# Kernel tuning notes

Hardware: AMD Instinct MI355X
Metric: run time of the kernel (lower is better)

The kernel has to match this reference:

```python
import jax, jax.numpy as jnp
import numpy as np

D_MODEL = 1024
N_HEADS = 16
N_KV = 4
HEAD_DIM = 64
R = 256
B, N = 2, 2048


def setup_inputs() -> dict:
    key = jax.random.key(0)
    ks = jax.random.split(key, 5)
    x = jax.random.normal(ks[0], (B, N, D_MODEL), jnp.float32)
    # rotary cos/sin table: (N, HEAD_DIM//2, 2)
    inv = 1.0 / (10000.0 ** (jnp.arange(0, HEAD_DIM, 2, dtype=jnp.float32) / HEAD_DIM))
    ang = jnp.arange(N, dtype=jnp.float32)[:, None] * inv[None, :]
    freqs_cis = jnp.stack([jnp.cos(ang), jnp.sin(ang)], axis=-1)
    s = 0.02
    Wq = jax.random.normal(ks[1], (D_MODEL, N_HEADS * HEAD_DIM), jnp.float32) * s
    Wk = jax.random.normal(ks[2], (D_MODEL, N_KV * HEAD_DIM), jnp.float32) * s
    Wv = jax.random.normal(ks[3], (D_MODEL, N_KV * HEAD_DIM), jnp.float32) * s
    Wo = jax.random.normal(ks[4], (N_HEADS * HEAD_DIM, D_MODEL), jnp.float32) * s
    return dict(x=x, freqs_cis=freqs_cis, Wq=Wq, Wk=Wk, Wv=Wv, Wo=Wo)


def _select_pairs(scores_i, best_b_i, r):
    """Greedy top-r pair selection with unique-b constraint (one batch row)."""
    half = scores_i.shape[0]
    order = jnp.argsort(-scores_i)  # descending by best similarity

    def step(carry, a_local):
        used, count = carry
        b_local = best_b_i[a_local]
        take = jnp.logical_and(jnp.logical_not(used[b_local]), count < r)
        used = used.at[b_local].set(used[b_local] | take)
        count = count + take.astype(jnp.int32)
        return (used, count), (take, a_local.astype(jnp.int32), b_local.astype(jnp.int32))

    (_, count), (takes, a_locs, b_locs) = jax.lax.scan(
        step, (jnp.zeros(half, bool), jnp.int32(0)), order)
    pos = jnp.cumsum(takes.astype(jnp.int32)) - 1
    idx = jnp.where(takes, pos, r)  # dump non-taken into slot r
    sel_a = jnp.zeros(r + 1, jnp.int32).at[idx].set(a_locs)[:r]
    sel_b = jnp.zeros(r + 1, jnp.int32).at[idx].set(b_locs)[:r]
    valid = jnp.arange(r) < count  # pad (if fewer than r unique) with first pair
    sel_a = jnp.where(valid, sel_a, sel_a[0])
    sel_b = jnp.where(valid, sel_b, sel_b[0])
    return sel_a, sel_b


def bipartite_indices(metric, r):
    """Returns (global_a, global_b, keep_idx) for merge/unmerge."""
    Bm, Nm, _ = metric.shape
    a = metric[:, 0::2]  # (B, half, C)
    b = metric[:, 1::2]
    an = a / jnp.maximum(jnp.linalg.norm(a, axis=-1, keepdims=True), 1e-12)
    bn = b / jnp.maximum(jnp.linalg.norm(b, axis=-1, keepdims=True), 1e-12)
    scores = jnp.einsum('bic,bjc->bij', an, bn)  # (B, half, half)
    best_scores = scores.max(axis=2)
    best_b = scores.argmax(axis=2)
    sel_a, sel_b = jax.vmap(lambda s, m: _select_pairs(s, m, r))(best_scores, best_b)
    global_a = 2 * sel_a      # even indices
    global_b = 2 * sel_b + 1  # odd indices
    bidx = jnp.arange(Bm)[:, None]
    keep_mask = jnp.ones((Bm, Nm), bool).at[bidx, global_b].set(False)
    # stable argsort puts kept (False) positions first, in original order
    keep_idx = jnp.argsort(~keep_mask, axis=1)[:, :Nm - r]
    return global_a, global_b, keep_idx


def merge(x, global_a, global_b, keep_idx):
    Bm = x.shape[0]
    bidx = jnp.arange(Bm)[:, None]
    xa = jnp.take_along_axis(x, global_a[..., None], axis=1)
    xb = jnp.take_along_axis(x, global_b[..., None], axis=1)
    x_out = x.at[bidx, global_a].set((xa + xb) * 0.5)
    return jnp.take_along_axis(x_out, keep_idx[..., None], axis=1)


def unmerge(xm, global_a, global_b, keep_idx, n_orig):
    Bm, _, C = xm.shape
    bidx = jnp.arange(Bm)[:, None]
    out = jnp.zeros((Bm, n_orig, C), xm.dtype).at[bidx, keep_idx].set(xm)
    xa = jnp.take_along_axis(out, global_a[..., None], axis=1)
    return out.at[bidx, global_b].set(xa)


def _rope(t, freqs):
    # t: (B, N, H, HD), freqs: (N, HD//2, 2)
    cos = freqs[None, :, None, :, 0]
    sin = freqs[None, :, None, :, 1]
    t1 = t[..., 0::2]
    t2 = t[..., 1::2]
    rot = jnp.stack([t1 * cos - t2 * sin, t1 * sin + t2 * cos], axis=-1)
    return rot.reshape(t.shape)


def _attention(x_m, freqs, Wq, Wk, Wv, Wo):
    Bm, Nm, _ = x_m.shape
    q = (x_m @ Wq).reshape(Bm, Nm, N_HEADS, HEAD_DIM)
    k = (x_m @ Wk).reshape(Bm, Nm, N_KV, HEAD_DIM)
    v = (x_m @ Wv).reshape(Bm, Nm, N_KV, HEAD_DIM)
    q = _rope(q, freqs)
    k = _rope(k, freqs)
    rep = N_HEADS // N_KV
    k = jnp.repeat(k, rep, axis=2)
    v = jnp.repeat(v, rep, axis=2)
    att = jnp.einsum('bqhd,bkhd->bhqk', q, k) / np.sqrt(HEAD_DIM).astype(np.float32)
    w = jax.nn.softmax(att, axis=-1)
    o = jnp.einsum('bhqk,bkhd->bqhd', w, v).reshape(Bm, Nm, N_HEADS * HEAD_DIM)
    return o @ Wo


def reference(x, freqs_cis, Wq, Wk, Wv, Wo):
    n = x.shape[1]
    metric = jax.lax.stop_gradient(x @ Wk)  # k_proj under no_grad
    ga, gb, ki = bipartite_indices(metric, R)
    x_m = merge(x, ga, gb, ki)
    n_merged = x_m.shape[1]
    out_m = _attention(x_m, freqs_cis[:n_merged], Wq, Wk, Wv, Wo)
    return unmerge(out_m, ga, gb, ki, n)
```

## Files before the change

kernel.cpp:

```cpp
#include <hip/hip_runtime.h>
#include <hip/hip_bf16.h>
#include <math.h>

#define BB 2
#define NN 2048
#define DM 1024
#define NH 16
#define NKV 4
#define HD 64
#define RR 256
#define HALF 1024
#define NM 1792
#define NT 28
#define NSPL 4

typedef __bf16 bf16x8 __attribute__((ext_vector_type(8)));
typedef float f32x4 __attribute__((ext_vector_type(4)));

__device__ inline unsigned pk2(float a, float b) {
  union { __bf16 h; unsigned short u; } ua, ub;
  ua.h = (__bf16)a;
  ub.h = (__bf16)b;
  return (unsigned)ua.u | ((unsigned)ub.u << 16);
}

__device__ inline unsigned shu(unsigned v, int s) {
  return (unsigned)__shfl((int)v, s, 64);
}

__global__ __launch_bounds__(256) void gemm_bf16(
    const __bf16* __restrict__ A, const __bf16* __restrict__ Bt,
    float* __restrict__ C, int M, int N, int K) {
  __shared__ __align__(16) __bf16 As[4096];
  __shared__ __align__(16) __bf16 Bs[4096];
  const int bm0 = blockIdx.x * 64;
  const int bn0 = blockIdx.y * 64;
  const int w = threadIdx.x >> 6;
  const int lane = threadIdx.x & 63;
  f32x4 acc[4];
#pragma unroll
  for (int nt = 0; nt < 4; ++nt) acc[nt] = (f32x4){0.f, 0.f, 0.f, 0.f};
  for (int kk = 0; kk < K; kk += 64) {
    __syncthreads();
#pragma unroll
    for (int t2 = threadIdx.x; t2 < 512; t2 += 256) {
      const int blk = t2 >> 7, s = (t2 >> 6) & 1, l = t2 & 63;
      const int kc = kk + s * 32 + ((l >> 4) << 3);
      *(float4*)&As[t2 * 8] =
          *(const float4*)(A + (size_t)(bm0 + blk * 16 + (l & 15)) * K + kc);
      *(float4*)&Bs[t2 * 8] =
          *(const float4*)(Bt + (size_t)(bn0 + blk * 16 + (l & 15)) * K + kc);
    }
    __syncthreads();
#pragma unroll
    for (int s = 0; s < 2; ++s) {
      bf16x8 a = *(const bf16x8*)&As[((w * 2 + s) * 64 + lane) * 8];
#pragma unroll
      for (int nt = 0; nt < 4; ++nt) {
        bf16x8 bfr = *(const bf16x8*)&Bs[((nt * 2 + s) * 64 + lane) * 8];
        acc[nt] =
            __builtin_amdgcn_mfma_f32_16x16x32_bf16(a, bfr, acc[nt], 0, 0, 0);
      }
    }
  }
  const int g = lane >> 4, ml = lane & 15;
#pragma unroll
  for (int nt = 0; nt < 4; ++nt)
#pragma unroll
    for (int r = 0; r < 4; ++r)
      C[(size_t)(bm0 + w * 16 + g * 4 + r) * N + bn0 + nt * 16 + ml] =
          acc[nt][r];
}

__global__ __launch_bounds__(256) void gemm_wo(
    const __bf16* __restrict__ A, const __bf16* __restrict__ Bt,
    const int* __restrict__ keep_idx, const int* __restrict__ dst2,
    float* __restrict__ out, int M, int N, int K) {
  __shared__ __align__(16) __bf16 As[4096];
  __shared__ __align__(16) __bf16 Bs[4096];
  const int bm0 = blockIdx.x * 64;
  const int bn0 = blockIdx.y * 64;
  const int w = threadIdx.x >> 6;
  const int lane = threadIdx.x & 63;
  f32x4 acc[4];
#pragma unroll
  for (int nt = 0; nt < 4; ++nt) acc[nt] = (f32x4){0.f, 0.f, 0.f, 0.f};
  for (int kk = 0; kk < K; kk += 64) {
    __syncthreads();
#pragma unroll
    for (int t2 = threadIdx.x; t2 < 512; t2 += 256) {
      const int blk = t2 >> 7, s = (t2 >> 6) & 1, l = t2 & 63;
      const int kc = kk + s * 32 + ((l >> 4) << 3);
      *(float4*)&As[t2 * 8] =
          *(const float4*)(A + (size_t)(bm0 + blk * 16 + (l & 15)) * K + kc);
      *(float4*)&Bs[t2 * 8] =
          *(const float4*)(Bt + (size_t)(bn0 + blk * 16 + (l & 15)) * K + kc);
    }
    __syncthreads();
#pragma unroll
    for (int s = 0; s < 2; ++s) {
      bf16x8 a = *(const bf16x8*)&As[((w * 2 + s) * 64 + lane) * 8];
#pragma unroll
      for (int nt = 0; nt < 4; ++nt) {
        bf16x8 bfr = *(const bf16x8*)&Bs[((nt * 2 + s) * 64 + lane) * 8];
        acc[nt] =
            __builtin_amdgcn_mfma_f32_16x16x32_bf16(a, bfr, acc[nt], 0, 0, 0);
      }
    }
  }
  const int g = lane >> 4, ml = lane & 15;
#pragma unroll
  for (int r = 0; r < 4; ++r) {
    const int row = bm0 + w * 16 + g * 4 + r;
    const int bb = row / NM, tt = row % NM;
    const int p1 = keep_idx[bb * NM + tt];
    const int p2 = dst2[bb * NM + tt];
#pragma unroll
    for (int nt = 0; nt < 4; ++nt) {
      const int col = bn0 + nt * 16 + ml;
      float v = acc[nt][r];
      out[((size_t)(bb * NN + p1)) * DM + col] = v;
      if (p2 >= 0) out[((size_t)(bb * NN + p2)) * DM + col] = v;
    }
  }
}

__global__ __launch_bounds__(256) void gemm3t(
    const __bf16* __restrict__ Ah, const __bf16* __restrict__ Al,
    const __bf16* __restrict__ Bh, const __bf16* __restrict__ Bl,
    float* __restrict__ C0, float* __restrict__ C1, int M, int N, int K) {
  __shared__ __align__(16) __bf16 Ahs[4096], Als[4096], Bhs[4096], Bls[4096];
  const int z = blockIdx.z;
  float* C = z ? C1 : C0;
  const int kof = z * (K / 2);
  const int bm0 = blockIdx.x * 64;
  const int bn0 = blockIdx.y * 64;
  const int w = threadIdx.x >> 6;
  const int lane = threadIdx.x & 63;
  f32x4 acc[4];
#pragma unroll
  for (int nt = 0; nt < 4; ++nt) acc[nt] = (f32x4){0.f, 0.f, 0.f, 0.f};
  for (int kk = kof; kk < kof + K / 2; kk += 64) {
    __syncthreads();
#pragma unroll
    for (int t2 = threadIdx.x; t2 < 512; t2 += 256) {
      const int blk = t2 >> 7, s = (t2 >> 6) & 1, l = t2 & 63;
      const size_t ra = (size_t)(bm0 + blk * 16 + (l & 15)) * K;
      const size_t rb = (size_t)(bn0 + blk * 16 + (l & 15)) * K;
      const int col = kk + s * 32 + ((l >> 4) << 3);
      *(float4*)&Ahs[t2 * 8] = *(const float4*)(Ah + ra + col);
      *(float4*)&Als[t2 * 8] = *(const float4*)(Al + ra + col);
      *(float4*)&Bhs[t2 * 8] = *(const float4*)(Bh + rb + col);
      *(float4*)&Bls[t2 * 8] = *(const float4*)(Bl + rb + col);
    }
    __syncthreads();
#pragma unroll
    for (int s = 0; s < 2; ++s) {
      bf16x8 ah = *(const bf16x8*)&Ahs[((w * 2 + s) * 64 + lane) * 8];
      bf16x8 al = *(const bf16x8*)&Als[((w * 2 + s) * 64 + lane) * 8];
#pragma unroll
      for (int nt = 0; nt < 4; ++nt) {
        bf16x8 bh = *(const bf16x8*)&Bhs[((nt * 2 + s) * 64 + lane) * 8];
        bf16x8 bl = *(const bf16x8*)&Bls[((nt * 2 + s) * 64 + lane) * 8];
        acc[nt] = __builtin_amdgcn_mfma_f32_16x16x32_bf16(al, bh, acc[nt], 0, 0, 0);
        acc[nt] = __builtin_amdgcn_mfma_f32_16x16x32_bf16(ah, bl, acc[nt], 0, 0, 0);
        acc[nt] = __builtin_amdgcn_mfma_f32_16x16x32_bf16(ah, bh, acc[nt], 0, 0, 0);
      }
    }
  }
  const int g = lane >> 4, ml = lane & 15;
#pragma unroll
  for (int nt = 0; nt < 4; ++nt)
#pragma unroll
    for (int r = 0; r < 4; ++r)
      C[(size_t)(bm0 + w * 16 + g * 4 + r) * N + bn0 + nt * 16 + ml] =
          acc[nt][r];
}

__global__ __launch_bounds__(256) void gemm_scam(
    const __bf16* __restrict__ Ah, const __bf16* __restrict__ Al,
    const __bf16* __restrict__ Bh, const __bf16* __restrict__ Bl,
    float* __restrict__ sval, int* __restrict__ sidx) {
  __shared__ __align__(16) __bf16 Ahs[4096], Als[4096], Bhs[4096], Bls[4096];
  const size_t zo = (size_t)blockIdx.z * HALF * 256;
  const int bm0 = blockIdx.x * 64;
  const int bn0 = blockIdx.y * 64;
  const int w = threadIdx.x >> 6;
  const int lane = threadIdx.x & 63;
  f32x4 acc[4];
#pragma unroll
  for (int nt = 0; nt < 4; ++nt) acc[nt] = (f32x4){0.f, 0.f, 0.f, 0.f};
  for (int kk = 0; kk < 256; kk += 64) {
    __syncthreads();
#pragma unroll
    for (int t2 = threadIdx.x; t2 < 512; t2 += 256) {
      const int blk = t2 >> 7, s = (t2 >> 6) & 1, l = t2 & 63;
      const size_t ra = zo + (size_t)(bm0 + blk * 16 + (l & 15)) * 256;
      const size_t rb = zo + (size_t)(bn0 + blk * 16 + (l & 15)) * 256;
      const int col = kk + s * 32 + ((l >> 4) << 3);
      *(float4*)&Ahs[t2 * 8] = *(const float4*)(Ah + ra + col);
      *(float4*)&Als[t2 * 8] = *(const float4*)(Al + ra + col);
      *(float4*)&Bhs[t2 * 8] = *(const float4*)(Bh + rb + col);
      *(float4*)&Bls[t2 * 8] = *(const float4*)(Bl + rb + col);
    }
    __syncthreads();
#pragma unroll
    for (int s = 0; s < 2; ++s) {
      bf16x8 ah = *(const bf16x8*)&Ahs[((w * 2 + s) * 64 + lane) * 8];
      bf16x8 al = *(const bf16x8*)&Als[((w * 2 + s) * 64 + lane) * 8];
#pragma unroll
      for (int nt = 0; nt < 4; ++nt) {
        bf16x8 bh = *(const bf16x8*)&Bhs[((nt * 2 + s) * 64 + lane) * 8];
        bf16x8 bl = *(const bf16x8*)&Bls[((nt * 2 + s) * 64 + lane) * 8];
        acc[nt] = __builtin_amdgcn_mfma_f32_16x16x32_bf16(al, bh, acc[nt], 0, 0, 0);
        acc[nt] = __builtin_amdgcn_mfma_f32_16x16x32_bf16(ah, bl, acc[nt], 0, 0, 0);
        acc[nt] = __builtin_amdgcn_mfma_f32_16x16x32_bf16(ah, bh, acc[nt], 0, 0, 0);
      }
    }
  }
  const int g = lane >> 4, ml = lane & 15;
#pragma unroll
  for (int r = 0; r < 4; ++r) {
    float bv = acc[0][r];
    int bc = bn0 + ml;
#pragma unroll
    for (int nt = 1; nt < 4; ++nt) {
      float v = acc[nt][r];
      int c = bn0 + nt * 16 + ml;
      if (v > bv) { bv = v; bc = c; }
    }
#pragma unroll
    for (int off = 1; off < 16; off <<= 1) {
      float vo = __shfl_xor(bv, off, 64);
      int co = __shfl_xor(bc, off, 64);
      if (vo > bv || (vo == bv && co < bc)) { bv = vo; bc = co; }
    }
    if (ml == 0) {
      const int row = bm0 + w * 16 + g * 4 + r;
      const size_t o = ((size_t)blockIdx.z * HALF + row) * 16 + (bn0 >> 6);
      sval[o] = bv;
      sidx[o] = bc;
    }
  }
}

__global__ __launch_bounds__(256) void argmax_reduce(
    const float* __restrict__ sval, const int* __restrict__ sidx,
    float* __restrict__ best_s, int* __restrict__ best_b) {
  const int lane = threadIdx.x & 63;
  const int e = lane & 15;
  const int rid = blockIdx.x * 16 + (threadIdx.x >> 6) * 4 + (lane >> 4);
  float bv = sval[rid * 16 + e];
  int bc = sidx[rid * 16 + e];
#pragma unroll
  for (int off = 1; off < 16; off <<= 1) {
    float vo = __shfl_xor(bv, off, 64);
    int co = __shfl_xor(bc, off, 64);
    if (vo > bv || (vo == bv && co < bc)) { bv = vo; bc = co; }
  }
  if (e == 0) {
    best_s[rid] = bv;
    best_b[rid] = bc;
  }
}

__global__ __launch_bounds__(256) void hilo_split(const float* __restrict__ x,
                                                  __bf16* __restrict__ xh,
                                                  __bf16* __restrict__ xl) {
  const int i = blockIdx.x * 256 + threadIdx.x;
  float4 v = ((const float4*)x)[i];
  float f[4] = {v.x, v.y, v.z, v.w};
  union { __bf16 h[4]; uint2 u; } H, L;
#pragma unroll
  for (int j = 0; j < 4; ++j) {
    __bf16 hh = (__bf16)f[j];
    H.h[j] = hh;
    L.h[j] = (__bf16)(f[j] - (float)hh);
  }
  ((uint2*)xh)[i] = H.u;
  ((uint2*)xl)[i] = L.u;
}

__global__ __launch_bounds__(256) void transpose_all(
    const float* __restrict__ Wq, const float* __restrict__ Wk,
    const float* __restrict__ Wv, const float* __restrict__ Wo,
    __bf16* __restrict__ Wqkvt, __bf16* __restrict__ Wktl,
    __bf16* __restrict__ Wot) {
  __shared__ float ld[64][65];
  const int z = blockIdx.x;
  const float* src;
  __bf16* dsth;
  __bf16* dstl = nullptr;
  int N, k0, n0, rowoff;
  if (z < 256) {
    src = Wq; N = 1024; k0 = (z >> 4) << 6; n0 = (z & 15) << 6;
    dsth = Wqkvt; rowoff = 0;
  } else if (z < 320) {
    int zz = z - 256;
    src = Wk; N = 256; k0 = (zz >> 2) << 6; n0 = (zz & 3) << 6;
    dsth = Wqkvt; rowoff = 1024; dstl = Wktl;
  } else if (z < 384) {
    int zz = z - 320;
    src = Wv; N = 256; k0 = (zz >> 2) << 6; n0 = (zz & 3) << 6;
    dsth = Wqkvt; rowoff = 1280;
  } else {
    int zz = z - 384;
    src = Wo; N = 1024; k0 = (zz >> 4) << 6; n0 = (zz & 15) << 6;
    dsth = Wot; rowoff = 0;
  }
  for (int i = threadIdx.x; i < 1024; i += 256) {
    int r = i >> 4, c4 = i & 15;
    float4 v = *(const float4*)(src + (size_t)(k0 + r) * N + n0 + c4 * 4);
    ld[r][c4 * 4 + 0] = v.x;
    ld[r][c4 * 4 + 1] = v.y;
    ld[r][c4 * 4 + 2] = v.z;
    ld[r][c4 * 4 + 3] = v.w;
  }
  __syncthreads();
  for (int i = threadIdx.x; i < 4096; i += 256) {
    int n = i >> 6, k = i & 63;
    float v = ld[k][n];
    __bf16 hh = (__bf16)v;
    dsth[(size_t)(rowoff + n0 + n) * 1024 + k0 + k] = hh;
    if (dstl)
      dstl[(size_t)(n0 + n) * 1024 + k0 + k] = (__bf16)(v - (float)hh);
  }
}

__global__ __launch_bounds__(256) void normalize_split(
    const float* __restrict__ m0, const float* __restrict__ m1,
    __bf16* __restrict__ anh, __bf16* __restrict__ anl,
    __bf16* __restrict__ bnh, __bf16* __restrict__ bnl) {
  const int row = blockIdx.x;
  const int b = row >> 11;
  const int r = row & 2047;
  const int t = threadIdx.x;
  float v = m0[(size_t)row * 256 + t] + m1[(size_t)row * 256 + t];
  float ss = v * v;
#pragma unroll
  for (int o = 32; o > 0; o >>= 1) ss += __shfl_xor(ss, o, 64);
  __shared__ float wsum[4];
  if ((t & 63) == 0) wsum[t >> 6] = ss;
  __syncthreads();
  float tot = wsum[0] + wsum[1] + wsum[2] + wsum[3];
  float inv = 1.f / fmaxf(sqrtf(tot), 1e-12f);
  float nv = v * inv;
  __bf16 hh = (__bf16)nv;
  __bf16 ll = (__bf16)(nv - (float)hh);
  size_t o = ((size_t)b * HALF + (r >> 1)) * 256 + t;
  if (r & 1) {
    bnh[o] = hh;
    bnl[o] = ll;
  } else {
    anh[o] = hh;
    anl[o] = ll;
  }
}

__global__ __launch_bounds__(512) void sort_desc(const float* __restrict__ best_s,
                                                 int* __restrict__ order) {
  const int b = blockIdx.x;
  __shared__ float sv[1024];
  __shared__ int si[1024];
  for (int i = threadIdx.x; i < 1024; i += 512) {
    sv[i] = best_s[b * HALF + i];
    si[i] = i;
  }
  __syncthreads();
  for (int k = 2; k <= 1024; k <<= 1) {
    for (int j = k >> 1; j > 0; j >>= 1) {
      for (int t = threadIdx.x; t < 1024; t += 512) {
        int ixj = t ^ j;
        if (ixj > t) {
          bool dir = ((t & k) == 0);
          float va = sv[t], vb = sv[ixj];
          int ia = si[t], ib = si[ixj];
          bool before = (vb > va) || (vb == va && ib < ia);
          if (before == dir) {
            sv[t] = vb; sv[ixj] = va;
            si[t] = ib; si[ixj] = ia;
          }
        }
      }
      __syncthreads();
    }
  }
  for (int i = threadIdx.x; i < 1024; i += 512) order[b * HALF + i] = si[i];
}

__global__ __launch_bounds__(256) void select_and_index(
    const int* __restrict__ best_b, const int* __restrict__ order,
    int* __restrict__ keep_idx, int* __restrict__ partner,
    int* __restrict__ dst2) {
  const int b = blockIdx.x;
  __shared__ int rankA[HALF];
  __shared__ int minrank[HALF];
  __shared__ int taken[HALF];
  __shared__ int sel_a[RR], sel_b[RR];
  __shared__ int removed[NN];
  __shared__ int src_row[NN];
  __shared__ int tsum[256];
  const int t = threadIdx.x;

  for (int i = t; i < HALF; i += 256) { minrank[i] = 0x7fffffff; taken[i] = 0; }
  for (int i = t; i < NN; i += 256) {
    removed[i] = 0;
    partner[b * NN + i] = -1;
  }
  for (int i = t; i < NM; i += 256) dst2[b * NM + i] = -1;
  __syncthreads();
  int ord[4];
#pragma unroll
  for (int q = 0; q < 4; ++q) {
    int step = t * 4 + q;
    ord[q] = order[b * HALF + step];
    rankA[ord[q]] = step;
  }
  __syncthreads();
#pragma unroll
  for (int q = 0; q < 4; ++q) {
    int a = t * 4 + q;
    atomicMin(&minrank[best_b[b * HALF + a]], rankA[a]);
  }
  __syncthreads();
  for (int i = t; i < HALF; i += 256) {
    int mr = minrank[i];
    if (mr != 0x7fffffff) taken[mr] = 1;
  }
  __syncthreads();
  int c[4];
  int mysum = 0;
#pragma unroll
  for (int q = 0; q < 4; ++q) { c[q] = taken[t * 4 + q]; mysum += c[q]; }
  tsum[t] = mysum;
  __syncthreads();
  for (int off = 1; off < 256; off <<= 1) {
    int v = (t >= off) ? tsum[t - off] : 0;
    __syncthreads();
    tsum[t] += v;
    __syncthreads();
  }
  int run = tsum[t] - mysum;
#pragma unroll
  for (int q = 0; q < 4; ++q) {
    if (c[q] && run < RR) {
      int a = ord[q];
      sel_a[run] = 2 * a;
      sel_b[run] = 2 * best_b[b * HALF + a] + 1;
    }
    run += c[q];
  }
  __syncthreads();
  const int cnt = min(tsum[255], RR);
  if (t >= cnt) { sel_a[t] = sel_a[0]; sel_b[t] = sel_b[0]; }
  __syncthreads();
  {
    int ga = sel_a[t], gb = sel_b[t];
    removed[gb] = 1;
    partner[b * NN + ga] = gb;
  }
  __syncthreads();
  int myc = 0;
#pragma unroll
  for (int q = 0; q < 8; ++q) myc += !removed[8 * t + q];
  tsum[t] = myc;
  __syncthreads();
  for (int off = 1; off < 256; off <<= 1) {
    int v = (t >= off) ? tsum[t - off] : 0;
    __syncthreads();
    tsum[t] += v;
    __syncthreads();
  }
  int pos = tsum[t] - myc;
#pragma unroll
  for (int q = 0; q < 8; ++q) {
    int p = 8 * t + q;
    int sr = -1;
    if (!removed[p]) {
      if (pos < NM) {
        keep_idx[b * NM + pos] = p;
        sr = pos;
      }
      ++pos;
    }
    src_row[p] = sr;
  }
  __syncthreads();
  {
    int sr = src_row[sel_a[t]];
    dst2[b * NM + sr] = sel_b[t];
  }
}

__global__ __launch_bounds__(256) void merge_kernel(
    const float* __restrict__ x, const int* __restrict__ keep_idx,
    const int* __restrict__ partner, __bf16* __restrict__ x_mb) {
  const int mrow = blockIdx.x;
  const int b = mrow / NM;
  const int t = mrow % NM;
  const int p = keep_idx[b * NM + t];
  const int pp = partner[b * NN + p];
  const float4* src =
      reinterpret_cast<const float4*>(x + ((size_t)b * NN + p) * DM);
  float4 val = src[threadIdx.x];
  if (pp >= 0) {
    const float4* s2 =
        reinterpret_cast<const float4*>(x + ((size_t)b * NN + pp) * DM);
    float4 v2 = s2[threadIdx.x];
    val.x = 0.5f * (val.x + v2.x);
    val.y = 0.5f * (val.y + v2.y);
    val.z = 0.5f * (val.z + v2.z);
    val.w = 0.5f * (val.w + v2.w);
  }
  union { __bf16 h[4]; uint2 u; } U;
  U.h[0] = (__bf16)val.x;
  U.h[1] = (__bf16)val.y;
  U.h[2] = (__bf16)val.z;
  U.h[3] = (__bf16)val.w;
  ((uint2*)(x_mb + (size_t)mrow * DM))[threadIdx.x] = U.u;
}

__global__ __launch_bounds__(256) void rope_fused(
    const float* __restrict__ qkv, const float* __restrict__ fc,
    __bf16* __restrict__ qbh, __bf16* __restrict__ kbh) {
  const int row = blockIdx.x;
  const int t = row % NM;
  const int b = row / NM;
  for (int idx = threadIdx.x; idx < 640; idx += 256) {
    int u = idx & 31;
    float c = fc[(t * 32 + u) * 2];
    float s = fc[(t * 32 + u) * 2 + 1];
    if (idx < 512) {
      int h = idx >> 5;
      const float* p = qkv + (size_t)row * 1536 + h * 64 + 2 * u;
      float x1 = p[0], x2 = p[1];
      __bf16* d = qbh + ((size_t)(b * NH + h) * NM + t) * 64 + 2 * u;
      d[0] = (__bf16)((x1 * c - x2 * s) * 0.125f);
      d[1] = (__bf16)((x1 * s + x2 * c) * 0.125f);
    } else {
      int h = (idx - 512) >> 5;
      const float* p = qkv + (size_t)row * 1536 + 1024 + h * 64 + 2 * u;
      float x1 = p[0], x2 = p[1];
      __bf16* d = kbh + ((size_t)(b * NKV + h) * NM + t) * 64 + 2 * u;
      d[0] = (__bf16)(x1 * c - x2 * s);
      d[1] = (__bf16)(x1 * s + x2 * c);
    }
  }
}

__global__ __launch_bounds__(256) void v_repack(const float* __restrict__ qkv,
                                                __bf16* __restrict__ vtb) {
  __shared__ float ld[64][65];
  int bid = blockIdx.x;
  const int kt = bid % (NM / 64); bid /= (NM / 64);
  const int kvh = bid % NKV;
  const int b = bid / NKV;
  const int j0 = kt * 64;
  for (int t2 = threadIdx.x; t2 < 1024; t2 += 256) {
    int key = t2 >> 4, c4 = t2 & 15;
    float4 v4 = *reinterpret_cast<const float4*>(
        qkv + (size_t)(b * NM + j0 + key) * 1536 + 1280 + kvh * 64 + c4 * 4);
    ld[key][c4 * 4 + 0] = v4.x;
    ld[key][c4 * 4 + 1] = v4.y;
    ld[key][c4 * 4 + 2] = v4.z;
    ld[key][c4 * 4 + 3] = v4.w;
  }
  __syncthreads();
  const int dim = threadIdx.x >> 2, kc = threadIdx.x & 3;
  __bf16* out = vtb + ((size_t)(b * NKV + kvh) * 64 + dim) * NM + j0 + kc * 16;
#pragma unroll
  for (int kk = 0; kk < 16; ++kk) out[kk] = (__bf16)ld[kc * 16 + kk][dim];
}

__global__ __launch_bounds__(512) void attn_mfma(
    const __bf16* __restrict__ qbh, const __bf16* __restrict__ kbh,
    const __bf16* __restrict__ vtb, float* __restrict__ pl,
    __bf16* __restrict__ pacc) {
  __shared__ __align__(16) __bf16 Ks[4096];
  __shared__ __align__(16) __bf16 Vs[4096];
  int bid = blockIdx.x;
  const int qt2 = bid % (NM / 32); bid /= (NM / 32);
  const int split = bid % NSPL; bid /= NSPL;
  const int kvh = bid % NKV;
  const int b = bid / NKV;
  const int w = threadIdx.x >> 6;
  const int lane = threadIdx.x & 63;
  const int h = kvh * 4 + (w & 3);
  const int qt = qt2 * 32 + (w >> 2) * 16;
  const int g = lane >> 4;
  const int ml = lane & 15;

  const __bf16* qrow = qbh + ((size_t)(b * NH + h) * NM + qt + ml) * 64;
  bf16x8 qa0 = *reinterpret_cast<const bf16x8*>(qrow + g * 8);
  bf16x8 qa1 = *reinterpret_cast<const bf16x8*>(qrow + 32 + g * 8);

  f32x4 acc[4];
#pragma unroll
  for (int mt = 0; mt < 4; ++mt) acc[mt] = (f32x4){0.f, 0.f, 0.f, 0.f};
  float lsum = 0.f;

  const __bf16* kp = kbh + (size_t)(b * NKV + kvh) * NM * 64;
  const __bf16* vp = vtb + (size_t)(b * NKV + kvh) * 64 * NM;
  const int src0 = ((lane >> 4) & 1) * 32 + ml;
  const int src1 = src0 + 16;
  const int sel = g >> 1;

  const int jt0 = split * (NT / NSPL);
  for (int jt = jt0; jt < jt0 + NT / NSPL; ++jt) {
    __syncthreads();
    {
      const int t2 = threadIdx.x;
      const int blk = t2 >> 7, s = (t2 >> 6) & 1, l = t2 & 63;
      *(float4*)&Ks[t2 * 8] = *(const float4*)(
          kp + (size_t)(jt * 64 + blk * 16 + (l & 15)) * 64 + s * 32 +
          ((l >> 4) << 3));
      *(float4*)&Vs[t2 * 8] = *(const float4*)(
          vp + (size_t)(blk * 16 + (l & 15)) * NM + jt * 64 + s * 32 +
          ((l >> 4) << 3));
    }
    __syncthreads();
    f32x4 S[4];
#pragma unroll
    for (int nt = 0; nt < 4; ++nt) {
      bf16x8 k0 = *(const bf16x8*)&Ks[(nt * 128 + lane) * 8];
      bf16x8 k1 = *(const bf16x8*)&Ks[(nt * 128 + 64 + lane) * 8];
      f32x4 s4 = (f32x4){0.f, 0.f, 0.f, 0.f};
      s4 = __builtin_amdgcn_mfma_f32_16x16x32_bf16(k0, qa0, s4, 0, 0, 0);
      s4 = __builtin_amdgcn_mfma_f32_16x16x32_bf16(k1, qa1, s4, 0, 0, 0);
      S[nt] = s4;
    }
    float p[4][4];
#pragma unroll
    for (int nt = 0; nt < 4; ++nt)
#pragma unroll
      for (int r = 0; r < 4; ++r) {
        p[nt][r] = __expf(S[nt][r]);
        lsum += p[nt][r];
      }
    unsigned pk[4][2];
#pragma unroll
    for (int nt = 0; nt < 4; ++nt) {
      pk[nt][0] = pk2(p[nt][0], p[nt][1]);
      pk[nt][1] = pk2(p[nt][2], p[nt][3]);
    }
    unsigned A00 = shu(pk[0][0], src0), A01 = shu(pk[0][1], src0);
    unsigned A10 = shu(pk[1][0], src0), A11 = shu(pk[1][1], src0);
    unsigned B00 = shu(pk[0][0], src1), B01 = shu(pk[0][1], src1);
    unsigned B10 = shu(pk[1][0], src1), B11 = shu(pk[1][1], src1);
    unsigned C00 = shu(pk[2][0], src0), C01 = shu(pk[2][1], src0);
    unsigned C10 = shu(pk[3][0], src0), C11 = shu(pk[3][1], src0);
    unsigned D00 = shu(pk[2][0], src1), D01 = shu(pk[2][1], src1);
    unsigned D10 = shu(pk[3][0], src1), D11 = shu(pk[3][1], src1);
    union { uint4 u; bf16x8 v; } P0, P1;
    P0.u.x = sel ? A10 : A00; P0.u.y = sel ? A11 : A01;
    P0.u.z = sel ? B10 : B00; P0.u.w = sel ? B11 : B01;
    P1.u.x = sel ? C10 : C00; P1.u.y = sel ? C11 : C01;
    P1.u.z = sel ? D10 : D00; P1.u.w = sel ? D11 : D01;
#pragma unroll
    for (int mt = 0; mt < 4; ++mt) {
      bf16x8 v0 = *(const bf16x8*)&Vs[(mt * 128 + lane) * 8];
      bf16x8 v1 = *(const bf16x8*)&Vs[(mt * 128 + 64 + lane) * 8];
      acc[mt] = __builtin_amdgcn_mfma_f32_16x16x32_bf16(v0, P0.v, acc[mt], 0, 0, 0);
      acc[mt] = __builtin_amdgcn_mfma_f32_16x16x32_bf16(v1, P1.v, acc[mt], 0, 0, 0);
    }
  }
  lsum += __shfl_xor(lsum, 16, 64);
  lsum += __shfl_xor(lsum, 32, 64);
  const size_t row = (size_t)(b * NH + h) * NM + qt + ml;
  if (g == 0) pl[row * NSPL + split] = lsum;
  __bf16* pa = pacc + (row * NSPL + split) * 64;
#pragma unroll
  for (int mt = 0; mt < 4; ++mt) {
    uint2 u;
    u.x = pk2(acc[mt][0], acc[mt][1]);
    u.y = pk2(acc[mt][2], acc[mt][3]);
    *reinterpret_cast<uint2*>(pa + mt * 16 + g * 4) = u;
  }
}

__global__ __launch_bounds__(256) void attn_combine(
    const float* __restrict__ pl, const __bf16* __restrict__ pacc,
    __bf16* __restrict__ attn_ob) {
  const size_t rid = (size_t)blockIdx.x * 4 + (threadIdx.x >> 6);
  const int d = threadIdx.x & 63;
  float num = 0.f, den = 0.f;
#pragma unroll
  for (int s = 0; s < NSPL; ++s) {
    num += (float)pacc[(rid * NSPL + s) * 64 + d];
    den += pl[rid * NSPL + s];
  }
  float o = num / den;
  const int q = (int)(rid % NM);
  const int h = (int)((rid / NM) % NH);
  const int b = (int)(rid / ((size_t)NM * NH));
  attn_ob[((size_t)(b * NM + q)) * DM + h * 64 + d] = (__bf16)o;
}

extern "C" void kernel_launch(void* const* d_in, const int* in_sizes, int n_in,
                              void* d_out, int out_size, void* d_ws,
                              size_t ws_size, hipStream_t stream) {
  const float* x = (const float*)d_in[0];
  const float* fc = (const float*)d_in[1];
  const float* Wq = (const float*)d_in[2];
  const float* Wk = (const float*)d_in[3];
  const float* Wv = (const float*)d_in[4];
  const float* Wo = (const float*)d_in[5];
  float* out = (float*)d_out;

  char* ws = (char*)d_ws;
  size_t off = 0;
  auto alloc = [&](size_t bytes) {
    void* p = ws + off;
    off += (bytes + 255) & ~(size_t)255;
    return p;
  };
  float* metric0 = (float*)alloc((size_t)BB * NN * 256 * 4);
  float* metric1 = (float*)alloc((size_t)BB * NN * 256 * 4);
  float* best_s = (float*)alloc((size_t)BB * HALF * 4);
  int* best_b = (int*)alloc((size_t)BB * HALF * 4);
  int* order = (int*)alloc((size_t)BB * HALF * 4);
  int* keep_idx = (int*)alloc((size_t)BB * NM * 4);
  int* partner = (int*)alloc((size_t)BB * NN * 4);
  int* dst2 = (int*)alloc((size_t)BB * NM * 4);
  float* sval = (float*)alloc((size_t)BB * HALF * 16 * 4);
  int* sidx = (int*)alloc((size_t)BB * HALF * 16 * 4);
  char* bigreg = (char*)alloc((size_t)30 * 1024 * 1024);
  __bf16* xh = (__bf16*)bigreg;
  __bf16* xl = (__bf16*)(bigreg + (size_t)8704 * 1024);
  __bf16* anh = (__bf16*)bigreg;
  __bf16* anl = (__bf16*)(bigreg + (size_t)1100 * 1024);
  __bf16* bnh = (__bf16*)(bigreg + (size_t)2200 * 1024);
  __bf16* bnl = (__bf16*)(bigreg + (size_t)3300 * 1024);
  float* qkv = (float*)bigreg;
  __bf16* pacc = (__bf16*)bigreg;
  __bf16* x_mb = (__bf16*)alloc((size_t)BB * NM * DM * 2);
  __bf16* qbh = (__bf16*)alloc((size_t)BB * NH * NM * 64 * 2);
  __bf16* kbh = (__bf16*)alloc((size_t)BB * NKV * NM * 64 * 2);
  __bf16* vtb = (__bf16*)alloc((size_t)BB * NKV * 64 * NM * 2);
  __bf16* attn_ob = (__bf16*)alloc((size_t)BB * NM * DM * 2);
  float* pl = (float*)alloc((size_t)BB * NH * NM * NSPL * 4);
  __bf16* Wqkvt = (__bf16*)alloc((size_t)1536 * DM * 2);
  __bf16* Wktl = (__bf16*)alloc((size_t)256 * DM * 2);
  __bf16* Wot = (__bf16*)alloc((size_t)DM * DM * 2);
  const __bf16* Wkth = Wqkvt + (size_t)1024 * 1024;

  transpose_all<<<640, 256, 0, stream>>>(Wq, Wk, Wv, Wo, Wqkvt, Wktl, Wot);
  hilo_split<<<(BB * NN * DM / 4) / 256, 256, 0, stream>>>(x, xh, xl);
  gemm3t<<<dim3(64, 4, 2), 256, 0, stream>>>(xh, xl, Wkth, Wktl, metric0,
                                             metric1, BB * NN, 256, DM);
  normalize_split<<<BB * NN, 256, 0, stream>>>(metric0, metric1, anh, anl, bnh,
                                               bnl);
  gemm_scam<<<dim3(16, 16, 2), 256, 0, stream>>>(anh, anl, bnh, bnl, sval,
                                                 sidx);
  argmax_reduce<<<(BB * HALF) / 16, 256, 0, stream>>>(sval, sidx, best_s,
                                                      best_b);
  sort_desc<<<BB, 512, 0, stream>>>(best_s, order);
  select_and_index<<<BB, 256, 0, stream>>>(best_b, order, keep_idx, partner,
                                           dst2);
  merge_kernel<<<BB * NM, 256, 0, stream>>>(x, keep_idx, partner, x_mb);
  gemm_bf16<<<dim3(56, 24), 256, 0, stream>>>(x_mb, Wqkvt, qkv, BB * NM, 1536,
                                              DM);
  rope_fused<<<BB * NM, 256, 0, stream>>>(qkv, fc, qbh, kbh);
  v_repack<<<BB * NKV * (NM / 64), 256, 0, stream>>>(qkv, vtb);
  attn_mfma<<<BB * NKV * NSPL * (NM / 32), 512, 0, stream>>>(qbh, kbh, vtb, pl,
                                                             pacc);
  attn_combine<<<(BB * NH * NM) / 4, 256, 0, stream>>>(pl, pacc, attn_ob);
  gemm_wo<<<dim3(56, 16), 256, 0, stream>>>(attn_ob, Wot, keep_idx, dst2, out,
                                            BB * NM, DM, DM);
}
```

Measured before the change: 306.6 us.

## Use async global-to-LDS loads and 128-row tiles in projection GEMMs

Replaces register-staged global-to-shared copies with `global_load_lds` direct-to-LDS transfers in all GEMM kernels and in the attention K/V tile loads. This is meant to remove the VGPR round trip and the extra LDS write instructions. The QKV and output-projection GEMMs also move to 128-row tiles with two accumulator sets per wave, so each B tile is reused twice and launch grids are halved. The trade-off is higher register and LDS use per block and fewer blocks to fill the GPU. There is still no double buffering, so load latency remains exposed behind the barriers.

```diff
diff --git a/kernel.cpp b/kernel.cpp
--- a/kernel.cpp
+++ b/kernel.cpp
@@ -28,101 +28,131 @@
   return (unsigned)__shfl((int)v, s, 64);
 }
 
+__device__ __forceinline__ void async16(const void* g, void* l) {
+  __builtin_amdgcn_global_load_lds(
+      (const __attribute__((address_space(1))) void*)g,
+      (__attribute__((address_space(3))) void*)l, 16, 0, 0);
+}
+
 __global__ __launch_bounds__(256) void gemm_bf16(
     const __bf16* __restrict__ A, const __bf16* __restrict__ Bt,
     float* __restrict__ C, int M, int N, int K) {
-  __shared__ __align__(16) __bf16 As[4096];
+  __shared__ __align__(16) __bf16 As[8192];
   __shared__ __align__(16) __bf16 Bs[4096];
-  const int bm0 = blockIdx.x * 64;
+  const int bm0 = blockIdx.x * 128;
   const int bn0 = blockIdx.y * 64;
   const int w = threadIdx.x >> 6;
   const int lane = threadIdx.x & 63;
-  f32x4 acc[4];
-#pragma unroll
-  for (int nt = 0; nt < 4; ++nt) acc[nt] = (f32x4){0.f, 0.f, 0.f, 0.f};
+  f32x4 acc[2][4];
+#pragma unroll
+  for (int i = 0; i < 2; ++i)
+#pragma unroll
+    for (int nt = 0; nt < 4; ++nt) acc[i][nt] = (f32x4){0.f, 0.f, 0.f, 0.f};
   for (int kk = 0; kk < K; kk += 64) {
     __syncthreads();
 #pragma unroll
-    for (int t2 = threadIdx.x; t2 < 512; t2 += 256) {
-      const int blk = t2 >> 7, s = (t2 >> 6) & 1, l = t2 & 63;
-      const int kc = kk + s * 32 + ((l >> 4) << 3);
-      *(float4*)&As[t2 * 8] =
-          *(const float4*)(A + (size_t)(bm0 + blk * 16 + (l & 15)) * K + kc);
-      *(float4*)&Bs[t2 * 8] =
-          *(const float4*)(Bt + (size_t)(bn0 + blk * 16 + (l & 15)) * K + kc);
+    for (int it = 0; it < 4; ++it) {
+      const int c = it * 256 + w * 64 + lane;
+      async16(A + (size_t)(bm0 + ((c >> 7) << 4) + (c & 15)) * K + kk +
+                  (((c >> 6) & 1) << 5) + (((c >> 4) & 3) << 3),
+              &As[(it * 256 + w * 64) * 8]);
+    }
+#pragma unroll
+    for (int it = 0; it < 2; ++it) {
+      const int c = it * 256 + w * 64 + lane;
+      async16(Bt + (size_t)(bn0 + ((c >> 7) << 4) + (c & 15)) * K + kk +
+                  (((c >> 6) & 1) << 5) + (((c >> 4) & 3) << 3),
+              &Bs[(it * 256 + w * 64) * 8]);
     }
     __syncthreads();
 #pragma unroll
     for (int s = 0; s < 2; ++s) {
-      bf16x8 a = *(const bf16x8*)&As[((w * 2 + s) * 64 + lane) * 8];
+      bf16x8 a0 = *(const bf16x8*)&As[((2 * w) * 128 + s * 64 + lane) * 8];
+      bf16x8 a1 = *(const bf16x8*)&As[((2 * w + 1) * 128 + s * 64 + lane) * 8];
 #pragma unroll
       for (int nt = 0; nt < 4; ++nt) {
-        bf16x8 bfr = *(const bf16x8*)&Bs[((nt * 2 + s) * 64 + lane) * 8];
-        acc[nt] =
-            __builtin_amdgcn_mfma_f32_16x16x32_bf16(a, bfr, acc[nt], 0, 0, 0);
+        bf16x8 bfr = *(const bf16x8*)&Bs[(nt * 128 + s * 64 + lane) * 8];
+        acc[0][nt] =
+            __builtin_amdgcn_mfma_f32_16x16x32_bf16(a0, bfr, acc[0][nt], 0, 0, 0);
+        acc[1][nt] =
+            __builtin_amdgcn_mfma_f32_16x16x32_bf16(a1, bfr, acc[1][nt], 0, 0, 0);
       }
     }
   }
   const int g = lane >> 4, ml = lane & 15;
 #pragma unroll
-  for (int nt = 0; nt < 4; ++nt)
-#pragma unroll
-    for (int r = 0; r < 4; ++r)
-      C[(size_t)(bm0 + w * 16 + g * 4 + r) * N + bn0 + nt * 16 + ml] =
-          acc[nt][r];
+  for (int i = 0; i < 2; ++i)
+#pragma unroll
+    for (int nt = 0; nt < 4; ++nt)
+#pragma unroll
+      for (int r = 0; r < 4; ++r)
+        C[(size_t)(bm0 + (2 * w + i) * 16 + g * 4 + r) * N + bn0 + nt * 16 +
+          ml] = acc[i][nt][r];
 }
 
 __global__ __launch_bounds__(256) void gemm_wo(
     const __bf16* __restrict__ A, const __bf16* __restrict__ Bt,
     const int* __restrict__ keep_idx, const int* __restrict__ dst2,
     float* __restrict__ out, int M, int N, int K) {
-  __shared__ __align__(16) __bf16 As[4096];
+  __shared__ __align__(16) __bf16 As[8192];
   __shared__ __align__(16) __bf16 Bs[4096];
-  const int bm0 = blockIdx.x * 64;
+  const int bm0 = blockIdx.x * 128;
   const int bn0 = blockIdx.y * 64;
   const int w = threadIdx.x >> 6;
   const int lane = threadIdx.x & 63;
-  f32x4 acc[4];
-#pragma unroll
-  for (int nt = 0; nt < 4; ++nt) acc[nt] = (f32x4){0.f, 0.f, 0.f, 0.f};
+  f32x4 acc[2][4];
+#pragma unroll
+  for (int i = 0; i < 2; ++i)
+#pragma unroll
+    for (int nt = 0; nt < 4; ++nt) acc[i][nt] = (f32x4){0.f, 0.f, 0.f, 0.f};
   for (int kk = 0; kk < K; kk += 64) {
     __syncthreads();
 #pragma unroll
-    for (int t2 = threadIdx.x; t2 < 512; t2 += 256) {
-      const int blk = t2 >> 7, s = (t2 >> 6) & 1, l = t2 & 63;
-      const int kc = kk + s * 32 + ((l >> 4) << 3);
-      *(float4*)&As[t2 * 8] =
-          *(const float4*)(A + (size_t)(bm0 + blk * 16 + (l & 15)) * K + kc);
-      *(float4*)&Bs[t2 * 8] =
-          *(const float4*)(Bt + (size_t)(bn0 + blk * 16 + (l & 15)) * K + kc);
+    for (int it = 0; it < 4; ++it) {
+      const int c = it * 256 + w * 64 + lane;
+      async16(A + (size_t)(bm0 + ((c >> 7) << 4) + (c & 15)) * K + kk +
+                  (((c >> 6) & 1) << 5) + (((c >> 4) & 3) << 3),
+              &As[(it * 256 + w * 64) * 8]);
+    }
+#pragma unroll
+    for (int it = 0; it < 2; ++it) {
+      const int c = it * 256 + w * 64 + lane;
+      async16(Bt + (size_t)(bn0 + ((c >> 7) << 4) + (c & 15)) * K + kk +
+                  (((c >> 6) & 1) << 5) + (((c >> 4) & 3) << 3),
+              &Bs[(it * 256 + w * 64) * 8]);
     }
     __syncthreads();
 #pragma unroll
     for (int s = 0; s < 2; ++s) {
-      bf16x8 a = *(const bf16x8*)&As[((w * 2 + s) * 64 + lane) * 8];
+      bf16x8 a0 = *(const bf16x8*)&As[((2 * w) * 128 + s * 64 + lane) * 8];
+      bf16x8 a1 = *(const bf16x8*)&As[((2 * w + 1) * 128 + s * 64 + lane) * 8];
 #pragma unroll
       for (int nt = 0; nt < 4; ++nt) {
-        bf16x8 bfr = *(const bf16x8*)&Bs[((nt * 2 + s) * 64 + lane) * 8];
-        acc[nt] =
-            __builtin_amdgcn_mfma_f32_16x16x32_bf16(a, bfr, acc[nt], 0, 0, 0);
+        bf16x8 bfr = *(const bf16x8*)&Bs[(nt * 128 + s * 64 + lane) * 8];
+        acc[0][nt] =
+            __builtin_amdgcn_mfma_f32_16x16x32_bf16(a0, bfr, acc[0][nt], 0, 0, 0);
+        acc[1][nt] =
+            __builtin_amdgcn_mfma_f32_16x16x32_bf16(a1, bfr, acc[1][nt], 0, 0, 0);
       }
     }
   }
   const int g = lane >> 4, ml = lane & 15;
 #pragma unroll
-  for (int r = 0; r < 4; ++r) {
-    const int row = bm0 + w * 16 + g * 4 + r;
-    const int bb = row / NM, tt = row % NM;
-    const int p1 = keep_idx[bb * NM + tt];
-    const int p2 = dst2[bb * NM + tt];
-#pragma unroll
-    for (int nt = 0; nt < 4; ++nt) {
-      const int col = bn0 + nt * 16 + ml;
-      float v = acc[nt][r];
-      out[((size_t)(bb * NN + p1)) * DM + col] = v;
-      if (p2 >= 0) out[((size_t)(bb * NN + p2)) * DM + col] = v;
-    }
-  }
+  for (int i = 0; i < 2; ++i)
+#pragma unroll
+    for (int r = 0; r < 4; ++r) {
+      const int row = bm0 + (2 * w + i) * 16 + g * 4 + r;
+      const int bb = row / NM, tt = row % NM;
+      const int p1 = keep_idx[bb * NM + tt];
+      const int p2 = dst2[bb * NM + tt];
+#pragma unroll
+      for (int nt = 0; nt < 4; ++nt) {
+        const int col = bn0 + nt * 16 + ml;
+        float v = acc[i][nt][r];
+        out[((size_t)(bb * NN + p1)) * DM + col] = v;
+        if (p2 >= 0) out[((size_t)(bb * NN + p2)) * DM + col] = v;
+      }
+    }
 }
 
 __global__ __launch_bounds__(256) void gemm3t(
@@ -143,15 +173,16 @@
   for (int kk = kof; kk < kof + K / 2; kk += 64) {
     __syncthreads();
 #pragma unroll
-    for (int t2 = threadIdx.x; t2 < 512; t2 += 256) {
-      const int blk = t2 >> 7, s = (t2 >> 6) & 1, l = t2 & 63;
-      const size_t ra = (size_t)(bm0 + blk * 16 + (l & 15)) * K;
-      const size_t rb = (size_t)(bn0 + blk * 16 + (l & 15)) * K;
-      const int col = kk + s * 32 + ((l >> 4) << 3);
-      *(float4*)&Ahs[t2 * 8] = *(const float4*)(Ah + ra + col);
-      *(float4*)&Als[t2 * 8] = *(const float4*)(Al + ra + col);
-      *(float4*)&Bhs[t2 * 8] = *(const float4*)(Bh + rb + col);
-      *(float4*)&Bls[t2 * 8] = *(const float4*)(Bl + rb + col);
+    for (int it = 0; it < 2; ++it) {
+      const int c = it * 256 + w * 64 + lane;
+      const size_t ra = (size_t)(bm0 + ((c >> 7) << 4) + (c & 15)) * K;
+      const size_t rb = (size_t)(bn0 + ((c >> 7) << 4) + (c & 15)) * K;
+      const int col = kk + (((c >> 6) & 1) << 5) + (((c >> 4) & 3) << 3);
+      const int lb = (it * 256 + w * 64) * 8;
+      async16(Ah + ra + col, &Ahs[lb]);
+      async16(Al + ra + col, &Als[lb]);
+      async16(Bh + rb + col, &Bhs[lb]);
+      async16(Bl + rb + col, &Bls[lb]);
     }
     __syncthreads();
 #pragma unroll
@@ -193,15 +224,16 @@
   for (int kk = 0; kk < 256; kk += 64) {
     __syncthreads();
 #pragma unroll
-    for (int t2 = threadIdx.x; t2 < 512; t2 += 256) {
-      const int blk = t2 >> 7, s = (t2 >> 6) & 1, l = t2 & 63;
-      const size_t ra = zo + (size_t)(bm0 + blk * 16 + (l & 15)) * 256;
-      const size_t rb = zo + (size_t)(bn0 + blk * 16 + (l & 15)) * 256;
-      const int col = kk + s * 32 + ((l >> 4) << 3);
-      *(float4*)&Ahs[t2 * 8] = *(const float4*)(Ah + ra + col);
-      *(float4*)&Als[t2 * 8] = *(const float4*)(Al + ra + col);
-      *(float4*)&Bhs[t2 * 8] = *(const float4*)(Bh + rb + col);
-      *(float4*)&Bls[t2 * 8] = *(const float4*)(Bl + rb + col);
+    for (int it = 0; it < 2; ++it) {
+      const int c = it * 256 + w * 64 + lane;
+      const size_t ra = zo + (size_t)(bm0 + ((c >> 7) << 4) + (c & 15)) * 256;
+      const size_t rb = zo + (size_t)(bn0 + ((c >> 7) << 4) + (c & 15)) * 256;
+      const int col = kk + (((c >> 6) & 1) << 5) + (((c >> 4) & 3) << 3);
+      const int lb = (it * 256 + w * 64) * 8;
+      async16(Ah + ra + col, &Ahs[lb]);
+      async16(Al + ra + col, &Als[lb]);
+      async16(Bh + rb + col, &Bhs[lb]);
+      async16(Bl + rb + col, &Bls[lb]);
     }
     __syncthreads();
 #pragma unroll
@@ -609,14 +641,14 @@
   for (int jt = jt0; jt < jt0 + NT / NSPL; ++jt) {
     __syncthreads();
     {
-      const int t2 = threadIdx.x;
-      const int blk = t2 >> 7, s = (t2 >> 6) & 1, l = t2 & 63;
-      *(float4*)&Ks[t2 * 8] = *(const float4*)(
-          kp + (size_t)(jt * 64 + blk * 16 + (l & 15)) * 64 + s * 32 +
-          ((l >> 4) << 3));
-      *(float4*)&Vs[t2 * 8] = *(const float4*)(
-          vp + (size_t)(blk * 16 + (l & 15)) * NM + jt * 64 + s * 32 +
-          ((l >> 4) << 3));
+      const int c = threadIdx.x;
+      const int lb = (w * 64) * 8;
+      async16(kp + (size_t)(jt * 64 + ((c >> 7) << 4) + (c & 15)) * 64 +
+                  (((c >> 6) & 1) << 5) + (((c >> 4) & 3) << 3),
+              &Ks[lb]);
+      async16(vp + (size_t)(((c >> 7) << 4) + (c & 15)) * NM + jt * 64 +
+                  (((c >> 6) & 1) << 5) + (((c >> 4) & 3) << 3),
+              &Vs[lb]);
     }
     __syncthreads();
     f32x4 S[4];
@@ -758,13 +790,13 @@
   select_and_index<<<BB, 256, 0, stream>>>(best_b, order, keep_idx, partner,
                                            dst2);
   merge_kernel<<<BB * NM, 256, 0, stream>>>(x, keep_idx, partner, x_mb);
-  gemm_bf16<<<dim3(56, 24), 256, 0, stream>>>(x_mb, Wqkvt, qkv, BB * NM, 1536,
+  gemm_bf16<<<dim3(28, 24), 256, 0, stream>>>(x_mb, Wqkvt, qkv, BB * NM, 1536,
                                               DM);
   rope_fused<<<BB * NM, 256, 0, stream>>>(qkv, fc, qbh, kbh);
   v_repack<<<BB * NKV * (NM / 64), 256, 0, stream>>>(qkv, vtb);
   attn_mfma<<<BB * NKV * NSPL * (NM / 32), 512, 0, stream>>>(qbh, kbh, vtb, pl,
                                                              pacc);
   attn_combine<<<(BB * NH * NM) / 4, 256, 0, stream>>>(pl, pacc, attn_ob);
-  gemm_wo<<<dim3(56, 16), 256, 0, stream>>>(attn_ob, Wot, keep_idx, dst2, out,
+  gemm_wo<<<dim3(28, 16), 256, 0, stream>>>(attn_ob, Wot, keep_idx, dst2, out,
                                             BB * NM, DM, DM);
 }
```

Result: faster. 283.6 us (-7.5%).
